# Kernel tuning notes

Hardware: AMD Instinct MI355X
Metric: run time of the kernel (lower is better)

Reference implementation:

```python
import jax, jax.numpy as jnp
import numpy as np

RADIUS = 400.0
FIELD = 8000.0  # um extent of slide coordinate field


def setup_inputs() -> dict:
    key = jax.random.key(0)
    ks = jax.random.split(key, 8)
    B, N, D, H, K = 4, 4096, 1536, 512, 8
    images = jax.random.normal(ks[0], (B, N, D), dtype=jnp.float32)
    positions = jax.random.uniform(ks[1], (B, N, 2), dtype=jnp.float32) * FIELD
    W_feat = jax.random.normal(ks[2], (D, H), dtype=jnp.float32) * (1.0 / np.sqrt(D))
    b_feat = jnp.zeros((H,), dtype=jnp.float32)
    W_pos = jax.random.normal(ks[3], (2, H), dtype=jnp.float32) * 0.5
    W_gnn = jax.random.normal(ks[4], (H, H), dtype=jnp.float32) * (1.0 / np.sqrt(H))
    W_self = jax.random.normal(ks[5], (H, H), dtype=jnp.float32) * (1.0 / np.sqrt(H))
    anchors = jax.random.normal(ks[6], (K, D), dtype=jnp.float32)
    return {"images": images, "positions": positions, "W_feat": W_feat,
            "b_feat": b_feat, "W_pos": W_pos, "W_gnn": W_gnn,
            "W_self": W_self, "anchors": anchors}


def _radius_adjacency(pos):
    # pos: (N, 2). Dense O(N^2) radius graph (mirrors torch.cdist + mask).
    sq = jnp.sum(pos * pos, axis=-1)                       # (N,)
    d2 = sq[:, None] + sq[None, :] - 2.0 * (pos @ pos.T)   # (N, N)
    mask = d2 < (RADIUS * RADIUS)
    N = pos.shape[0]
    mask = mask & ~jnp.eye(N, dtype=bool)                  # no self-loops
    return mask.astype(pos.dtype)


def reference(images, positions, W_feat, b_feat, W_pos, W_gnn, W_self, anchors):
    # --- Stream A: explicit concept quantifier (cosine sim to anchors) ---
    x_norm = images / jnp.clip(jnp.linalg.norm(images, axis=-1, keepdims=True), 1e-12)
    a_norm = anchors / jnp.clip(jnp.linalg.norm(anchors, axis=-1, keepdims=True), 1e-12)
    scores = jnp.einsum('bnd,kd->bnk', x_norm, a_norm)     # (B, N, K)
    concept_profile = scores.mean(axis=1)                  # (B, K)

    # --- Stream B: feature extraction with positional encoding ---
    feat = images @ W_feat + b_feat + positions @ W_pos    # (B, N, H)

    # --- radius graph + one mean-aggregation GNN layer, per slide ---
    def per_graph(f, p):
        A = _radius_adjacency(p)                           # (N, N)
        deg = jnp.clip(A.sum(axis=-1, keepdims=True), 1.0) # (N, 1)
        h = jax.nn.relu(f)
        agg = (A @ h) / deg                                # mean over neighbors
        return jax.nn.relu(agg @ W_gnn + f @ W_self)       # (N, H)

    refined = jax.vmap(per_graph)(feat, positions)         # (B, N, H)
    latent_spatial = refined.mean(axis=1)                  # (B, H)  per-graph mean pool

    return jnp.concatenate([latent_spatial, concept_profile], axis=1)  # (B, H+K)
```

## Files before the change

kernel.cpp:

```cpp
#include <hip/hip_runtime.h>

#define B_ 4
#define N_ 4096
#define D_ 1536
#define H_ 512
#define K_ 8
#define M_ (B_*N_)
#define R2_ 160000.0f
#define CAP 192

typedef __attribute__((ext_vector_type(8))) short bf16x8;
typedef __attribute__((ext_vector_type(4))) float f32x4;
typedef __attribute__((ext_vector_type(2))) float f32x2;

__device__ __forceinline__ unsigned short f2bf(float f) {
  union { float f; unsigned u; } v; v.f = f;
  unsigned r = (v.u + 0x7FFFu + ((v.u >> 16) & 1u)) >> 16;
  return (unsigned short)r;
}

typedef const __attribute__((address_space(1))) unsigned int gas_u32;
typedef __attribute__((address_space(3))) unsigned int las_u32;
__device__ __forceinline__ void gl_lds16(const unsigned short* g, unsigned short* l) {
  __builtin_amdgcn_global_load_lds((gas_u32*)g, (las_u32*)l, 16, 0, 0);
}

__global__ __launch_bounds__(256) void k_prep(
    const float* __restrict__ Wf, const float* __restrict__ Wg, const float* __restrict__ Ws,
    const float* __restrict__ anchors, unsigned short* __restrict__ WfT,
    unsigned short* __restrict__ WgsT, float* __restrict__ anorm) {
  __shared__ float t[64][65];
  __shared__ float red[4];
  int bx = blockIdx.x, by = blockIdx.y, tid = threadIdx.x;
  if (by == 40) {
    int k = bx;
    float s = 0.f;
    for (int i = tid; i < D_; i += 256) { float v = anchors[k*D_ + i]; s += v*v; }
    #pragma unroll
    for (int off = 32; off; off >>= 1) s += __shfl_down(s, off);
    if ((tid & 63) == 0) red[tid >> 6] = s;
    __syncthreads();
    if (tid == 0) anorm[k] = fmaxf(sqrtf(red[0]+red[1]+red[2]+red[3]), 1e-12f);
    return;
  }
  const float* W; unsigned short* WT; int kt, outStride, outOff;
  if (by < 24)      { W = Wf; WT = WfT;  kt = by;      outStride = D_;   outOff = 0; }
  else if (by < 32) { W = Wg; WT = WgsT; kt = by - 24; outStride = 1024; outOff = 0; }
  else              { W = Ws; WT = WgsT; kt = by - 32; outStride = 1024; outOff = 512; }
  int tx = tid & 63, ty = tid >> 6;
  #pragma unroll
  for (int r = 0; r < 64; r += 4)
    t[ty + r][tx] = W[(size_t)(kt*64 + ty + r)*H_ + bx*64 + tx];
  __syncthreads();
  #pragma unroll
  for (int r = 0; r < 64; r += 4) {
    int n = bx*64 + ty + r;
    WT[(size_t)n*outStride + outOff + kt*64 + tx] = f2bf(t[tx][ty + r]);
  }
}

__global__ __launch_bounds__(256) void k_concept_cast(
    const float* __restrict__ images, const float* __restrict__ anchors,
    const float* __restrict__ anorm, unsigned short* __restrict__ imgs_bf,
    float* __restrict__ out) {
  __shared__ unsigned short sAb[K_*D_];
  __shared__ float sc[4][K_];
  int tid = threadIdx.x, lane = tid & 63, w = tid >> 6;
  {
    const float4* a4 = (const float4*)anchors;
    #pragma unroll
    for (int i = 0; i < 12; i++) {
      float4 a = a4[tid + 256*i];
      ushort4 s; s.x = f2bf(a.x); s.y = f2bf(a.y); s.z = f2bf(a.z); s.w = f2bf(a.w);
      ((ushort4*)sAb)[tid + 256*i] = s;
    }
  }
  __syncthreads();
  float acc_k[K_] = {};
  for (int r = 0; r < 4; r++) {
    int gm = blockIdx.x*16 + w*4 + r;
    const float4* xrow = (const float4*)(images + (size_t)gm*D_);
    float nrm = 0.f; float dot[K_] = {};
    #pragma unroll
    for (int it = 0; it < 6; it++) {
      int j = lane + 64*it;
      float4 x = xrow[j];
      nrm += x.x*x.x + x.y*x.y + x.z*x.z + x.w*x.w;
      #pragma unroll
      for (int k = 0; k < K_; k++) {
        uint2 a = *(const uint2*)&sAb[k*D_ + j*4];
        union { unsigned u; float f; } c;
        float s = 0.f;
        c.u = a.x << 16;         s += x.x*c.f;
        c.u = a.x & 0xFFFF0000u; s += x.y*c.f;
        c.u = a.y << 16;         s += x.z*c.f;
        c.u = a.y & 0xFFFF0000u; s += x.w*c.f;
        dot[k] += s;
      }
      ushort4 s;
      s.x = f2bf(x.x); s.y = f2bf(x.y); s.z = f2bf(x.z); s.w = f2bf(x.w);
      *(ushort4*)&imgs_bf[(size_t)gm*D_ + (size_t)j*4] = s;
    }
    #pragma unroll
    for (int off = 32; off; off >>= 1) {
      nrm += __shfl_down(nrm, off);
      #pragma unroll
      for (int k = 0; k < K_; k++) dot[k] += __shfl_down(dot[k], off);
    }
    if (lane == 0) {
      float inv = 1.0f / fmaxf(sqrtf(nrm), 1e-12f);
      #pragma unroll
      for (int k = 0; k < K_; k++) acc_k[k] += dot[k] * inv / anorm[k];
    }
  }
  if (lane == 0) {
    #pragma unroll
    for (int k = 0; k < K_; k++) sc[w][k] = acc_k[k];
  }
  __syncthreads();
  if (tid < K_) {
    float s = sc[0][tid] + sc[1][tid] + sc[2][tid] + sc[3][tid];
    int b = blockIdx.x >> 8;
    atomicAdd(out + b*(H_+K_) + H_ + tid, s * (1.0f/N_));
  }
}

#define BM 128
#define BN 128
#define BK 32

__global__ __launch_bounds__(256) void k_gemm(
    const unsigned short* __restrict__ A, const unsigned short* __restrict__ BT,
    int Kdim, int mode, const float* __restrict__ bias, const float* __restrict__ Wpos,
    const float* __restrict__ positions, unsigned short* __restrict__ AB,
    float* __restrict__ out) {
  __shared__ unsigned short As[BM*BK];
  __shared__ unsigned short Bs[BN*BK];
  __shared__ float colsum[BN];
  int tid = threadIdx.x;
  int lane = tid & 63, wv = tid >> 6;
  int wm = wv >> 1, wn = wv & 1;
  int l15 = lane & 15, quad = lane >> 4;
  int bx = blockIdx.x;
  int bm = bx >> 2, bn = bx & 3;
  int m0 = bm*BM, n0 = bn*BN;

  f32x4 acc[4][4] = {};

  int c = wv*2;
  int rowc = (lane >> 2), seg = lane & 3;
  const unsigned short* gA0 = A  + (size_t)(m0 + c*16 + rowc)*Kdim + seg*8;
  const unsigned short* gA1 = gA0 + (size_t)16*Kdim;
  const unsigned short* gB0 = BT + (size_t)(n0 + c*16 + rowc)*Kdim + seg*8;
  const unsigned short* gB1 = gB0 + (size_t)16*Kdim;
  unsigned short* lA0 = As + c*512;
  unsigned short* lA1 = lA0 + 512;
  unsigned short* lB0 = Bs + c*512;
  unsigned short* lB1 = lB0 + 512;

  int nk = Kdim / BK;
  for (int kt = 0; kt < nk; kt++) {
    __syncthreads();
    gl_lds16(gA0, lA0); gl_lds16(gA1, lA1);
    gl_lds16(gB0, lB0); gl_lds16(gB1, lB1);
    gA0 += BK; gA1 += BK; gB0 += BK; gB1 += BK;
    __syncthreads();

    bf16x8 aF[4], bF[4];
    #pragma unroll
    for (int f = 0; f < 4; f++)
      aF[f] = *(const bf16x8*)&As[(wm*64 + f*16 + l15)*BK + quad*8];
    #pragma unroll
    for (int f = 0; f < 4; f++)
      bF[f] = *(const bf16x8*)&Bs[(wn*64 + f*16 + l15)*BK + quad*8];
    #pragma unroll
    for (int mi = 0; mi < 4; mi++)
      #pragma unroll
      for (int ni = 0; ni < 4; ni++)
        acc[mi][ni] = __builtin_amdgcn_mfma_f32_16x16x32_bf16(aF[mi], bF[ni], acc[mi][ni], 0, 0, 0);
  }

  if (mode == 0) {
    float bz[4], w0v[4], w1v[4];
    #pragma unroll
    for (int ni = 0; ni < 4; ni++) {
      int gh = n0 + wn*64 + ni*16 + l15;
      bz[ni] = bias[gh]; w0v[ni] = Wpos[gh]; w1v[ni] = Wpos[H_ + gh];
    }
    #pragma unroll
    for (int mi = 0; mi < 4; mi++) {
      #pragma unroll
      for (int r = 0; r < 4; r++) {
        int gm = m0 + wm*64 + mi*16 + quad*4 + r;
        float2 p = ((const float2*)positions)[gm];
        #pragma unroll
        for (int ni = 0; ni < 4; ni++) {
          int gh = n0 + wn*64 + ni*16 + l15;
          float v = acc[mi][ni][r] + bz[ni] + p.x*w0v[ni] + p.y*w1v[ni];
          AB[(size_t)gm*1024 + 512 + gh] = f2bf(v);
        }
      }
    }
  } else {
    if (tid < BN) colsum[tid] = 0.f;
    __syncthreads();
    #pragma unroll
    for (int ni = 0; ni < 4; ni++) {
      float s = 0.f;
      #pragma unroll
      for (int mi = 0; mi < 4; mi++) {
        #pragma unroll
        for (int r = 0; r < 4; r++) s += fmaxf(acc[mi][ni][r], 0.f);
      }
      s += __shfl_down(s, 32);
      s += __shfl_down(s, 16);
      if (quad == 0) atomicAdd(&colsum[wn*64 + ni*16 + l15], s);
    }
    __syncthreads();
    if (tid < BN) {
      int b = m0 >> 12;
      atomicAdd(out + b*(H_+K_) + n0 + tid, colsum[tid] * (1.0f/N_));
    }
  }
}

__global__ __launch_bounds__(256) void k_quant(const unsigned short* __restrict__ AB,
                                               unsigned char* __restrict__ P) {
  int g = blockIdx.x*256 + threadIdx.x;
  int row = g >> 6, cg = (g & 63)*8;
  uint4 v = *(const uint4*)(AB + (size_t)row*1024 + 512 + cg);
  float f[8];
  union { unsigned u; float x; } t;
  t.u = v.x << 16; f[0]=t.x; t.u = v.x & 0xFFFF0000u; f[1]=t.x;
  t.u = v.y << 16; f[2]=t.x; t.u = v.y & 0xFFFF0000u; f[3]=t.x;
  t.u = v.z << 16; f[4]=t.x; t.u = v.z & 0xFFFF0000u; f[5]=t.x;
  t.u = v.w << 16; f[6]=t.x; t.u = v.w & 0xFFFF0000u; f[7]=t.x;
  #pragma unroll
  for (int i = 0; i < 8; i++) f[i] = fminf(fmaxf(f[i], 0.f)*0.015625f, 448.f);
  int u0 = __builtin_amdgcn_cvt_pk_fp8_f32(f[0], f[1], 0, false);
  u0     = __builtin_amdgcn_cvt_pk_fp8_f32(f[2], f[3], u0, true);
  int u1 = __builtin_amdgcn_cvt_pk_fp8_f32(f[4], f[5], 0, false);
  u1     = __builtin_amdgcn_cvt_pk_fp8_f32(f[6], f[7], u1, true);
  uint2 o; o.x = (unsigned)u0; o.y = (unsigned)u1;
  *(uint2*)(P + (size_t)row*512 + cg) = o;
}

__device__ __forceinline__ void accf8(uint2 v, float* a) {
  f32x2 p;
  p = __builtin_amdgcn_cvt_pk_f32_fp8(v.x, false); a[0] += p[0]; a[1] += p[1];
  p = __builtin_amdgcn_cvt_pk_f32_fp8(v.x, true);  a[2] += p[0]; a[3] += p[1];
  p = __builtin_amdgcn_cvt_pk_f32_fp8(v.y, false); a[4] += p[0]; a[5] += p[1];
  p = __builtin_amdgcn_cvt_pk_f32_fp8(v.y, true);  a[6] += p[0]; a[7] += p[1];
}

__global__ __launch_bounds__(256) void k_aggregate(const float* __restrict__ positions,
                                                   const unsigned char* __restrict__ P,
                                                   unsigned short* __restrict__ AB) {
  __shared__ unsigned short nl[8*CAP];
  __shared__ int cnt[8];
  __shared__ float sdx[8], sdy[8];
  int blk = blockIdx.x;
  int xcd = blk & 7;
  int b = xcd >> 1;
  int sub = ((blk >> 3) << 1) | (xcd & 1);
  int dest0 = sub * 8;
  int tid = threadIdx.x, lane = tid & 63, w = tid >> 6;
  const float2* p2 = (const float2*)(positions + (size_t)b*N_*2);
  if (tid < 8) {
    cnt[tid] = 0;
    float2 pd = p2[dest0 + tid];
    sdx[tid] = pd.x; sdy[tid] = pd.y;
  }
  __syncthreads();
  for (int it = 0; it < 16; it++) {
    int j = tid + 256*it;
    float2 pj = p2[j];
    #pragma unroll
    for (int d = 0; d < 8; d++) {
      float dx = pj.x - sdx[d], dy = pj.y - sdy[d];
      if (dx*dx + dy*dy < R2_ && j != dest0 + d) {
        int p = atomicAdd(&cnt[d], 1);
        if (p < CAP) nl[d*CAP + p] = (unsigned short)j;
      }
    }
  }
  __syncthreads();
  const unsigned char* featb = P + ((size_t)(b << 12))*512 + lane*8;
  #pragma unroll
  for (int dd = 0; dd < 2; dd++) {
    int d = w*2 + dd;
    int deg = cnt[d]; if (deg > CAP) deg = CAP;
    float inv = 64.0f / (float)(deg > 1 ? deg : 1);
    const unsigned short* nlp = &nl[d*CAP];
    float a[8] = {};
    int n = 0;
    for (; n + 4 <= deg; n += 4) {
      ushort4 idx = *(const ushort4*)&nlp[n];
      uint2 v0 = *(const uint2*)(featb + (size_t)idx.x*512);
      uint2 v1 = *(const uint2*)(featb + (size_t)idx.y*512);
      uint2 v2 = *(const uint2*)(featb + (size_t)idx.z*512);
      uint2 v3 = *(const uint2*)(featb + (size_t)idx.w*512);
      accf8(v0, a); accf8(v1, a); accf8(v2, a); accf8(v3, a);
    }
    for (; n < deg; n++) {
      int j = nlp[n];
      uint2 v = *(const uint2*)(featb + (size_t)j*512);
      accf8(v, a);
    }
    uint4 o;
    o.x = ((unsigned)f2bf(a[1]*inv) << 16) | f2bf(a[0]*inv);
    o.y = ((unsigned)f2bf(a[3]*inv) << 16) | f2bf(a[2]*inv);
    o.z = ((unsigned)f2bf(a[5]*inv) << 16) | f2bf(a[4]*inv);
    o.w = ((unsigned)f2bf(a[7]*inv) << 16) | f2bf(a[6]*inv);
    *(uint4*)(AB + (size_t)((b << 12) + dest0 + d)*1024 + lane*8) = o;
  }
}

extern "C" void kernel_launch(void* const* d_in, const int* in_sizes, int n_in,
                              void* d_out, int out_size, void* d_ws, size_t ws_size,
                              hipStream_t stream) {
  const float* images    = (const float*)d_in[0];
  const float* positions = (const float*)d_in[1];
  const float* W_feat    = (const float*)d_in[2];
  const float* b_feat    = (const float*)d_in[3];
  const float* W_pos     = (const float*)d_in[4];
  const float* W_gnn     = (const float*)d_in[5];
  const float* W_self    = (const float*)d_in[6];
  const float* anchors   = (const float*)d_in[7];
  float* out = (float*)d_out;

  char* ws = (char*)d_ws;
  unsigned short* imgs_bf = (unsigned short*)ws;
  unsigned char*  P       = (unsigned char*)ws;
  unsigned short* AB      = (unsigned short*)(ws + 50331648);
  unsigned short* WfT     = (unsigned short*)(ws + 83886080);
  unsigned short* WgsT    = (unsigned short*)(ws + 85458944);
  float*          anorm   = (float*)(ws + 86507520);

  hipMemsetAsync(d_out, 0, sizeof(float)*B_*(H_+K_), stream);
  k_prep<<<dim3(8, 41), 256, 0, stream>>>(W_feat, W_gnn, W_self, anchors, WfT, WgsT, anorm);
  k_concept_cast<<<M_/16, 256, 0, stream>>>(images, anchors, anorm, imgs_bf, out);
  k_gemm<<<512, 256, 0, stream>>>(imgs_bf, WfT, D_, 0, b_feat, W_pos, positions, AB, out);
  k_quant<<<4096, 256, 0, stream>>>(AB, P);
  k_aggregate<<<2048, 256, 0, stream>>>(positions, P, AB);
  k_gemm<<<512, 256, 0, stream>>>(AB, WgsT, 1024, 1, nullptr, nullptr, nullptr, AB, out);
}
```

Baseline: 290.6 us.

## Fuse prep into concept kernel and fold fp8 quantization into GEMM epilogue

Merges the weight-transpose/anchor-norm prep kernel and the concept/cast kernel into one launch, with each concept block computing anchor norms locally. The first GEMM's epilogue now restages outputs through LDS to write vectorized bf16 and also emits the fp8 relu-scaled copy directly, which removes the separate quantize kernel and its re-read of AB. P moves to its own workspace region because it is now written while imgs_bf is still live. Costs are an extra LDS round-trip and a barrier in the epilogue, plus redundant anchor-norm work in every concept block.

```diff
diff --git a/kernel.cpp b/kernel.cpp
--- a/kernel.cpp
+++ b/kernel.cpp
@@ -25,47 +25,41 @@
   __builtin_amdgcn_global_load_lds((gas_u32*)g, (las_u32*)l, 16, 0, 0);
 }
 
-__global__ __launch_bounds__(256) void k_prep(
+#define CONCEPT_BLKS 1024
+
+__global__ __launch_bounds__(256) void k_front(
+    const float* __restrict__ images, const float* __restrict__ anchors,
     const float* __restrict__ Wf, const float* __restrict__ Wg, const float* __restrict__ Ws,
-    const float* __restrict__ anchors, unsigned short* __restrict__ WfT,
-    unsigned short* __restrict__ WgsT, float* __restrict__ anorm) {
-  __shared__ float t[64][65];
-  __shared__ float red[4];
-  int bx = blockIdx.x, by = blockIdx.y, tid = threadIdx.x;
-  if (by == 40) {
-    int k = bx;
-    float s = 0.f;
-    for (int i = tid; i < D_; i += 256) { float v = anchors[k*D_ + i]; s += v*v; }
-    #pragma unroll
-    for (int off = 32; off; off >>= 1) s += __shfl_down(s, off);
-    if ((tid & 63) == 0) red[tid >> 6] = s;
-    __syncthreads();
-    if (tid == 0) anorm[k] = fmaxf(sqrtf(red[0]+red[1]+red[2]+red[3]), 1e-12f);
+    unsigned short* __restrict__ imgs_bf, unsigned short* __restrict__ WfT,
+    unsigned short* __restrict__ WgsT, float* __restrict__ out) {
+  __shared__ __align__(16) char smem[24832];
+  int tid = threadIdx.x;
+
+  if (blockIdx.x >= CONCEPT_BLKS) {
+    float (*t)[65] = (float(*)[65])smem;
+    int bi = blockIdx.x - CONCEPT_BLKS;
+    int bx = bi & 7, by = bi >> 3;
+    const float* W; unsigned short* WT; int kt, outStride, outOff;
+    if (by < 24)      { W = Wf; WT = WfT;  kt = by;      outStride = D_;   outOff = 0; }
+    else if (by < 32) { W = Wg; WT = WgsT; kt = by - 24; outStride = 1024; outOff = 0; }
+    else              { W = Ws; WT = WgsT; kt = by - 32; outStride = 1024; outOff = 512; }
+    int tx = tid & 63, ty = tid >> 6;
+    #pragma unroll
+    for (int r = 0; r < 64; r += 4)
+      t[ty + r][tx] = W[(size_t)(kt*64 + ty + r)*H_ + bx*64 + tx];
+    __syncthreads();
+    #pragma unroll
+    for (int r = 0; r < 64; r += 4) {
+      int n = bx*64 + ty + r;
+      WT[(size_t)n*outStride + outOff + kt*64 + tx] = f2bf(t[tx][ty + r]);
+    }
     return;
   }
-  const float* W; unsigned short* WT; int kt, outStride, outOff;
-  if (by < 24)      { W = Wf; WT = WfT;  kt = by;      outStride = D_;   outOff = 0; }
-  else if (by < 32) { W = Wg; WT = WgsT; kt = by - 24; outStride = 1024; outOff = 0; }
-  else              { W = Ws; WT = WgsT; kt = by - 32; outStride = 1024; outOff = 512; }
-  int tx = tid & 63, ty = tid >> 6;
-  #pragma unroll
-  for (int r = 0; r < 64; r += 4)
-    t[ty + r][tx] = W[(size_t)(kt*64 + ty + r)*H_ + bx*64 + tx];
-  __syncthreads();
-  #pragma unroll
-  for (int r = 0; r < 64; r += 4) {
-    int n = bx*64 + ty + r;
-    WT[(size_t)n*outStride + outOff + kt*64 + tx] = f2bf(t[tx][ty + r]);
-  }
-}
-
-__global__ __launch_bounds__(256) void k_concept_cast(
-    const float* __restrict__ images, const float* __restrict__ anchors,
-    const float* __restrict__ anorm, unsigned short* __restrict__ imgs_bf,
-    float* __restrict__ out) {
-  __shared__ unsigned short sAb[K_*D_];
-  __shared__ float sc[4][K_];
-  int tid = threadIdx.x, lane = tid & 63, w = tid >> 6;
+
+  unsigned short* sAb = (unsigned short*)smem;
+  float (*sc)[K_]    = (float(*)[K_])(smem + 24576);
+  float* sAnormInv   = (float*)(smem + 24704);
+  int lane = tid & 63, w = tid >> 6;
   {
     const float4* a4 = (const float4*)anchors;
     #pragma unroll
@@ -74,6 +68,16 @@
       ushort4 s; s.x = f2bf(a.x); s.y = f2bf(a.y); s.z = f2bf(a.z); s.w = f2bf(a.w);
       ((ushort4*)sAb)[tid + 256*i] = s;
     }
+  }
+  {
+    int k = tid >> 5, sl = tid & 31;
+    const float* ak = anchors + (size_t)k*D_;
+    float s = 0.f;
+    #pragma unroll 8
+    for (int i = 0; i < 48; i++) { float v = ak[sl + 32*i]; s += v*v; }
+    #pragma unroll
+    for (int off = 16; off; off >>= 1) s += __shfl_down(s, off, 32);
+    if (sl == 0) sAnormInv[k] = 1.0f / fmaxf(sqrtf(s), 1e-12f);
   }
   __syncthreads();
   float acc_k[K_] = {};
@@ -110,7 +114,7 @@
     if (lane == 0) {
       float inv = 1.0f / fmaxf(sqrtf(nrm), 1e-12f);
       #pragma unroll
-      for (int k = 0; k < K_; k++) acc_k[k] += dot[k] * inv / anorm[k];
+      for (int k = 0; k < K_; k++) acc_k[k] += dot[k] * inv * sAnormInv[k];
     }
   }
   if (lane == 0) {
@@ -133,8 +137,8 @@
     const unsigned short* __restrict__ A, const unsigned short* __restrict__ BT,
     int Kdim, int mode, const float* __restrict__ bias, const float* __restrict__ Wpos,
     const float* __restrict__ positions, unsigned short* __restrict__ AB,
-    float* __restrict__ out) {
-  __shared__ unsigned short As[BM*BK];
+    unsigned char* __restrict__ P, float* __restrict__ out) {
+  __shared__ __align__(16) unsigned short As[BM*BK];
   __shared__ unsigned short Bs[BN*BK];
   __shared__ float colsum[BN];
   int tid = threadIdx.x;
@@ -187,6 +191,9 @@
       int gh = n0 + wn*64 + ni*16 + l15;
       bz[ni] = bias[gh]; w0v[ni] = Wpos[gh]; w1v[ni] = Wpos[H_ + gh];
     }
+    __syncthreads();
+    float* sb = ((float*)As) + wv*256;
+    int col4 = n0 + wn*64 + l15*4;
     #pragma unroll
     for (int mi = 0; mi < 4; mi++) {
       #pragma unroll
@@ -195,10 +202,21 @@
         float2 p = ((const float2*)positions)[gm];
         #pragma unroll
         for (int ni = 0; ni < 4; ni++) {
-          int gh = n0 + wn*64 + ni*16 + l15;
           float v = acc[mi][ni][r] + bz[ni] + p.x*w0v[ni] + p.y*w1v[ni];
-          AB[(size_t)gm*1024 + 512 + gh] = f2bf(v);
+          sb[quad*64 + ni*16 + l15] = v;
         }
+        f32x4 q = *(f32x4*)&sb[quad*64 + l15*4];
+        uint2 o;
+        o.x = ((unsigned)f2bf(q[1]) << 16) | f2bf(q[0]);
+        o.y = ((unsigned)f2bf(q[3]) << 16) | f2bf(q[2]);
+        *(uint2*)&AB[(size_t)gm*1024 + 512 + col4] = o;
+        float e0 = fminf(fmaxf(q[0], 0.f)*0.015625f, 448.f);
+        float e1 = fminf(fmaxf(q[1], 0.f)*0.015625f, 448.f);
+        float e2 = fminf(fmaxf(q[2], 0.f)*0.015625f, 448.f);
+        float e3 = fminf(fmaxf(q[3], 0.f)*0.015625f, 448.f);
+        int u = __builtin_amdgcn_cvt_pk_fp8_f32(e0, e1, 0, false);
+        u     = __builtin_amdgcn_cvt_pk_fp8_f32(e2, e3, u, true);
+        *(unsigned*)(P + (size_t)gm*512 + col4) = (unsigned)u;
       }
     }
   } else {
@@ -222,27 +240,6 @@
       atomicAdd(out + b*(H_+K_) + n0 + tid, colsum[tid] * (1.0f/N_));
     }
   }
-}
-
-__global__ __launch_bounds__(256) void k_quant(const unsigned short* __restrict__ AB,
-                                               unsigned char* __restrict__ P) {
-  int g = blockIdx.x*256 + threadIdx.x;
-  int row = g >> 6, cg = (g & 63)*8;
-  uint4 v = *(const uint4*)(AB + (size_t)row*1024 + 512 + cg);
-  float f[8];
-  union { unsigned u; float x; } t;
-  t.u = v.x << 16; f[0]=t.x; t.u = v.x & 0xFFFF0000u; f[1]=t.x;
-  t.u = v.y << 16; f[2]=t.x; t.u = v.y & 0xFFFF0000u; f[3]=t.x;
-  t.u = v.z << 16; f[4]=t.x; t.u = v.z & 0xFFFF0000u; f[5]=t.x;
-  t.u = v.w << 16; f[6]=t.x; t.u = v.w & 0xFFFF0000u; f[7]=t.x;
-  #pragma unroll
-  for (int i = 0; i < 8; i++) f[i] = fminf(fmaxf(f[i], 0.f)*0.015625f, 448.f);
-  int u0 = __builtin_amdgcn_cvt_pk_fp8_f32(f[0], f[1], 0, false);
-  u0     = __builtin_amdgcn_cvt_pk_fp8_f32(f[2], f[3], u0, true);
-  int u1 = __builtin_amdgcn_cvt_pk_fp8_f32(f[4], f[5], 0, false);
-  u1     = __builtin_amdgcn_cvt_pk_fp8_f32(f[6], f[7], u1, true);
-  uint2 o; o.x = (unsigned)u0; o.y = (unsigned)u1;
-  *(uint2*)(P + (size_t)row*512 + cg) = o;
 }
 
 __device__ __forceinline__ void accf8(uint2 v, float* a) {
@@ -331,17 +328,15 @@
 
   char* ws = (char*)d_ws;
   unsigned short* imgs_bf = (unsigned short*)ws;
-  unsigned char*  P       = (unsigned char*)ws;
   unsigned short* AB      = (unsigned short*)(ws + 50331648);
   unsigned short* WfT     = (unsigned short*)(ws + 83886080);
   unsigned short* WgsT    = (unsigned short*)(ws + 85458944);
-  float*          anorm   = (float*)(ws + 86507520);
+  unsigned char*  P       = (unsigned char*)(ws + 86507520);
 
   hipMemsetAsync(d_out, 0, sizeof(float)*B_*(H_+K_), stream);
-  k_prep<<<dim3(8, 41), 256, 0, stream>>>(W_feat, W_gnn, W_self, anchors, WfT, WgsT, anorm);
-  k_concept_cast<<<M_/16, 256, 0, stream>>>(images, anchors, anorm, imgs_bf, out);
-  k_gemm<<<512, 256, 0, stream>>>(imgs_bf, WfT, D_, 0, b_feat, W_pos, positions, AB, out);
-  k_quant<<<4096, 256, 0, stream>>>(AB, P);
+  k_front<<<CONCEPT_BLKS + 320, 256, 0, stream>>>(images, anchors, W_feat, W_gnn, W_self,
+                                                  imgs_bf, WfT, WgsT, out);
+  k_gemm<<<512, 256, 0, stream>>>(imgs_bf, WfT, D_, 0, b_feat, W_pos, positions, AB, P, out);
   k_aggregate<<<2048, 256, 0, stream>>>(positions, P, AB);
-  k_gemm<<<512, 256, 0, stream>>>(AB, WgsT, 1024, 1, nullptr, nullptr, nullptr, AB, out);
-}
+  k_gemm<<<512, 256, 0, stream>>>(AB, WgsT, 1024, 1, nullptr, nullptr, nullptr, AB, nullptr, out);
+}
```

After: 331.3 us. +14.0%, slower.
